# Performance work log

Measured on AMD Instinct MI355X. Metric: run time of the kernel, lower is better.

The kernel has to match this reference:

```python
import jax, jax.numpy as jnp
import numpy as np
from jax import lax

N_NODES = 100000
N_EDGES = 1600000
DIM = 64
N_GRAPHS = 128
OUT = 10
BN_EPS = 1e-5


def setup_inputs() -> dict:
    key = jax.random.key(0)
    ks = jax.random.split(key, 8)
    s = 1.0 / np.sqrt(DIM)
    x = jax.random.normal(ks[0], (N_NODES, DIM), dtype=jnp.float32)
    edge_index = jax.random.randint(ks[1], (2, N_EDGES), 0, N_NODES, dtype=jnp.int64)
    batch = jnp.sort(jax.random.randint(ks[2], (N_NODES,), 0, N_GRAPHS, dtype=jnp.int64))
    return {
        "x": x,
        "edge_index": edge_index,
        "batch": batch,
        "W1": jax.random.normal(ks[3], (5, DIM, DIM), dtype=jnp.float32) * s,
        "b1": jnp.zeros((5, DIM), jnp.float32),
        "gamma": jnp.ones((5, DIM), jnp.float32),
        "beta": jnp.zeros((5, DIM), jnp.float32),
        "rmean": jnp.zeros((5, DIM), jnp.float32),
        "rvar": jnp.ones((5, DIM), jnp.float32),
        "W2": jax.random.normal(ks[4], (5, DIM, DIM), dtype=jnp.float32) * s,
        "b2": jnp.zeros((5, DIM), jnp.float32),
        "lin1_w": jax.random.normal(ks[5], (DIM, DIM), dtype=jnp.float32) * s,
        "lin1_b": jnp.zeros((DIM,), jnp.float32),
        "lin2_w": jax.random.normal(ks[6], (DIM, OUT), dtype=jnp.float32) * s,
        "lin2_b": jnp.zeros((OUT,), jnp.float32),
    }


def reference(x, edge_index, batch, W1, b1, gamma, beta, rmean, rvar, W2, b2,
              lin1_w, lin1_b, lin2_w, lin2_b):
    n = x.shape[0]
    src, dst = edge_index[0], edge_index[1]

    def gin_layer(h, p):
        w1, bb1, g, bt, m, v, w2, bb2 = p
        # GINConv (eps=0): h_i <- MLP(h_i + sum_{j in N(i)} h_j)
        agg = jax.ops.segment_sum(h[src], dst, num_segments=n)
        h = h + agg
        h = h @ w1 + bb1
        h = (h - m) * lax.rsqrt(v + BN_EPS) * g + bt  # BatchNorm1d (eval)
        h = jax.nn.relu(h)
        h = jax.nn.relu(h @ w2 + bb2)
        return h, None

    h, _ = lax.scan(gin_layer, x, (W1, b1, gamma, beta, rmean, rvar, W2, b2))
    # global_add_pool over graphs in the batch
    pooled = jax.ops.segment_sum(h, batch, num_segments=N_GRAPHS)  # [G, dim]
    pooled = jax.nn.relu(pooled @ lin1_w + lin1_b)
    # dropout is identity in eval mode
    return pooled @ lin2_w + lin2_b  # [G, out]
```

## Files before the change

### kernel.cpp

```cpp
#include <hip/hip_runtime.h>

#define N_NODES  100000
#define N_EDGES  1600000
#define DIM      64
#define N_GRAPHS 128
#define OUT_DIM  10
#define SCAN_NB    196
#define SCAN_CHUNK 512
#define RANGE_BITS 14
#define RANGE_SIZE 16384
#define N_RANGES   7
#define N_CHUNKS   32
#define CHUNK_EDGES (N_EDGES / N_CHUNKS)
#define NODE_PAD   (N_RANGES * RANGE_SIZE)

typedef unsigned int uint;
typedef unsigned short ushort;
typedef __attribute__((ext_vector_type(8))) short short8;
typedef __attribute__((ext_vector_type(4))) float f32x4;

__device__ __forceinline__ uint f2bf(float x) {
    uint b = __float_as_uint(x);
    b += 0x7fffu + ((b >> 16) & 1u);
    return b >> 16;
}


__global__ __launch_bounds__(1024) void histo_kernel(const int* __restrict__ dst,
                                                     int* __restrict__ counts8) {
    __shared__ int lds[RANGE_SIZE];
    const int r = blockIdx.x & 7;
    if (r >= N_RANGES) return;
    const int c = blockIdx.x >> 3;
    for (int j = threadIdx.x; j < RANGE_SIZE; j += 1024) lds[j] = 0;
    __syncthreads();
    const int beg = c * CHUNK_EDGES, end = beg + CHUNK_EDGES;
    for (int i = beg + threadIdx.x; i < end; i += 1024) {
        int d = dst[i];
        if ((d >> RANGE_BITS) == r) atomicAdd(&lds[d & (RANGE_SIZE - 1)], 1);
    }
    __syncthreads();
    int* outp = counts8 + (c * N_RANGES + r) * RANGE_SIZE;
    for (int j = threadIdx.x; j < RANGE_SIZE; j += 1024) outp[j] = lds[j];
}

__global__ void scanA_kernel(const int* __restrict__ counts8, int* __restrict__ blockSums, int n) {
    __shared__ int red[256];
    const int b = blockIdx.x, t = threadIdx.x;
    int s = 0;
#pragma unroll
    for (int k = 0; k < 2; ++k) {
        const int node = b * SCAN_CHUNK + t * 2 + k;
        if (node < n) {
            const int r = node >> RANGE_BITS, jj = node & (RANGE_SIZE - 1);
            for (int c = 0; c < N_CHUNKS; ++c)
                s += counts8[(c * N_RANGES + r) * RANGE_SIZE + jj];
        }
    }
    red[t] = s;
    __syncthreads();
    for (int off = 128; off > 0; off >>= 1) {
        if (t < off) red[t] += red[t + off];
        __syncthreads();
    }
    if (t == 0) blockSums[b] = red[0];
}

__global__ void scanB_kernel(const int* __restrict__ blockSums, int* __restrict__ blockOffs,
                             int* __restrict__ row_ptr) {
    __shared__ int sc[256];
    const int t = threadIdx.x;
    const int v = (t < SCAN_NB) ? blockSums[t] : 0;
    sc[t] = v;
    __syncthreads();
    for (int off = 1; off < 256; off <<= 1) {
        int u = (t >= off) ? sc[t - off] : 0;
        __syncthreads();
        sc[t] += u;
        __syncthreads();
    }
    if (t < SCAN_NB) blockOffs[t] = sc[t] - v;
    if (t == 255) row_ptr[N_NODES] = sc[255];
}

__global__ void scanC_kernel(const int* __restrict__ counts8, const int* __restrict__ blockOffs,
                             int* __restrict__ row_ptr, int* __restrict__ base8, int n) {
    __shared__ int sc[256];
    const int b = blockIdx.x, t = threadIdx.x;
    const int node0 = b * SCAN_CHUNK + t * 2;
    int cnt0[N_CHUNKS], cnt1[N_CHUNKS];
    int tot0 = 0, tot1 = 0;
    if (node0 < n) {
        const int r = node0 >> RANGE_BITS, jj = node0 & (RANGE_SIZE - 1);
        for (int c = 0; c < N_CHUNKS; ++c) {
            cnt0[c] = counts8[(c * N_RANGES + r) * RANGE_SIZE + jj];
            tot0 += cnt0[c];
        }
    }
    if (node0 + 1 < n) {
        const int r = (node0 + 1) >> RANGE_BITS, jj = (node0 + 1) & (RANGE_SIZE - 1);
        for (int c = 0; c < N_CHUNKS; ++c) {
            cnt1[c] = counts8[(c * N_RANGES + r) * RANGE_SIZE + jj];
            tot1 += cnt1[c];
        }
    }
    const int s = tot0 + tot1;
    sc[t] = s;
    __syncthreads();
    for (int off = 1; off < 256; off <<= 1) {
        int u = (t >= off) ? sc[t - off] : 0;
        __syncthreads();
        sc[t] += u;
        __syncthreads();
    }
    const int pre = blockOffs[b] + sc[t] - s;
    if (node0 < n) {
        row_ptr[node0] = pre;
        int run = pre;
        for (int c = 0; c < N_CHUNKS; ++c) { base8[c * NODE_PAD + node0] = run; run += cnt0[c]; }
    }
    if (node0 + 1 < n) {
        const int pre1 = pre + tot0;
        row_ptr[node0 + 1] = pre1;
        int run = pre1;
        for (int c = 0; c < N_CHUNKS; ++c) { base8[c * NODE_PAD + node0 + 1] = run; run += cnt1[c]; }
    }
}

__global__ __launch_bounds__(1024) void fill_kernel(const int* __restrict__ src,
                                                    const int* __restrict__ dst,
                                                    const int* __restrict__ base8,
                                                    int* __restrict__ col_idx) {
    __shared__ int lds[RANGE_SIZE];
    const int r = blockIdx.x & 7;
    if (r >= N_RANGES) return;
    const int c = blockIdx.x >> 3;
    const int* bp = base8 + c * NODE_PAD + r * RANGE_SIZE;
    for (int j = threadIdx.x; j < RANGE_SIZE; j += 1024) lds[j] = bp[j];
    __syncthreads();
    const int beg = c * CHUNK_EDGES, end = beg + CHUNK_EDGES;
    for (int i = beg + threadIdx.x; i < end; i += 1024) {
        int d = dst[i];
        if ((d >> RANGE_BITS) == r) {
            int pos = atomicAdd(&lds[d & (RANGE_SIZE - 1)], 1);
            col_idx[pos] = src[i];
        }
    }
}


__global__ void cvt_kernel(const float* __restrict__ x, ushort* __restrict__ xb, int n4) {
    int idx = blockIdx.x * blockDim.x + threadIdx.x;
    if (idx >= n4) return;
    float4 v = ((const float4*)x)[idx];
    uint2 o;
    o.x = f2bf(v.x) | (f2bf(v.y) << 16);
    o.y = f2bf(v.z) | (f2bf(v.w) << 16);
    ((uint2*)xb)[idx] = o;
}


__global__ void repack_kernel(const float* __restrict__ W1, const float* __restrict__ W2,
                              uint4* __restrict__ Wp) {
    const int wave = (blockIdx.x * blockDim.x + threadIdx.x) >> 6;
    if (wave >= 10) return;
    const int layer = wave >> 1;
    const float* W = (wave & 1) ? (W2 + layer * 4096) : (W1 + layer * 4096);
    const int lane = threadIdx.x & 63;
    const int n15 = lane & 15, quad = lane >> 4;
#pragma unroll
    for (int f = 0; f < 8; ++f) {
        const int outer = f >> 1, h = f & 1;
        uint p[4];
#pragma unroll
        for (int pj = 0; pj < 4; ++pj) {
            const int k0 = h * 32 + quad * 8 + 2 * pj;
            uint lo = f2bf(W[k0 * 64 + outer * 16 + n15]);
            uint hi = f2bf(W[(k0 + 1) * 64 + outer * 16 + n15]);
            p[pj] = lo | (hi << 16);
        }
        Wp[(wave * 8 + f) * 64 + lane] = make_uint4(p[0], p[1], p[2], p[3]);
    }
}


__device__ __forceinline__ void add_unpack(float acc[8], uint4 v) {
    acc[0] += __uint_as_float(v.x << 16);
    acc[1] += __uint_as_float(v.x & 0xffff0000u);
    acc[2] += __uint_as_float(v.y << 16);
    acc[3] += __uint_as_float(v.y & 0xffff0000u);
    acc[4] += __uint_as_float(v.z << 16);
    acc[5] += __uint_as_float(v.z & 0xffff0000u);
    acc[6] += __uint_as_float(v.w << 16);
    acc[7] += __uint_as_float(v.w & 0xffff0000u);
}

__global__ __launch_bounds__(256) void agg_kernel(
    const ushort* __restrict__ hb, ushort* __restrict__ tb,
    const int* __restrict__ row_ptr, const int* __restrict__ col_idx, int n)
{
    const uint4* __restrict__ hb4 = (const uint4*)hb;
    const int lane = threadIdx.x & 63;
    const int g = lane >> 3;
    const int q = lane & 7;
    const int wave = (blockIdx.x * blockDim.x + threadIdx.x) >> 6;
    const int i = wave * 8 + g;
    if (i >= n) return;
    const int rp0 = row_ptr[i];
    const int deg = row_ptr[i + 1] - rp0;

    float acc[8];
    {
        uint4 v = hb4[(size_t)i * 8 + q];
        acc[0] = __uint_as_float(v.x << 16);
        acc[1] = __uint_as_float(v.x & 0xffff0000u);
        acc[2] = __uint_as_float(v.y << 16);
        acc[3] = __uint_as_float(v.y & 0xffff0000u);
        acc[4] = __uint_as_float(v.z << 16);
        acc[5] = __uint_as_float(v.z & 0xffff0000u);
        acc[6] = __uint_as_float(v.w << 16);
        acc[7] = __uint_as_float(v.w & 0xffff0000u);
    }

    int e = 0;
    for (; e + 8 <= deg; e += 8) {
        int ix[8];
#pragma unroll
        for (int k = 0; k < 8; ++k) ix[k] = col_idx[rp0 + e + k];
        uint4 v[8];
#pragma unroll
        for (int k = 0; k < 8; ++k) v[k] = hb4[(size_t)ix[k] * 8 + q];
#pragma unroll
        for (int k = 0; k < 8; ++k) add_unpack(acc, v[k]);
    }
    if (e + 4 <= deg) {
        int ix[4];
#pragma unroll
        for (int k = 0; k < 4; ++k) ix[k] = col_idx[rp0 + e + k];
        uint4 v[4];
#pragma unroll
        for (int k = 0; k < 4; ++k) v[k] = hb4[(size_t)ix[k] * 8 + q];
#pragma unroll
        for (int k = 0; k < 4; ++k) add_unpack(acc, v[k]);
        e += 4;
    }
    for (; e < deg; ++e) {
        int ix = col_idx[rp0 + e];
        uint4 v = hb4[(size_t)ix * 8 + q];
        add_unpack(acc, v);
    }

    uint4 o;
    o.x = f2bf(acc[0]) | (f2bf(acc[1]) << 16);
    o.y = f2bf(acc[2]) | (f2bf(acc[3]) << 16);
    o.z = f2bf(acc[4]) | (f2bf(acc[5]) << 16);
    o.w = f2bf(acc[6]) | (f2bf(acc[7]) << 16);
    ((uint4*)tb)[(size_t)i * 8 + q] = o;
}


__global__ __launch_bounds__(256) void mlp_kernel(
    const ushort* __restrict__ tb, ushort* __restrict__ hb,
    const uint4* __restrict__ Wp,
    const float* __restrict__ b1, const float* __restrict__ gamma,
    const float* __restrict__ beta, const float* __restrict__ rmean,
    const float* __restrict__ rvar, const float* __restrict__ b2, int ntiles)
{
    __shared__ __align__(16) ushort U[4][16][72];
    const int lane = threadIdx.x & 63;
    const int wid  = threadIdx.x >> 6;
    const int n15  = lane & 15, quad = lane >> 4;

    short8 w1f[8], w2f[8];
    const short8* Wp8 = (const short8*)Wp;
#pragma unroll
    for (int f = 0; f < 8; ++f) {
        w1f[f] = Wp8[f * 64 + lane];
        w2f[f] = Wp8[(8 + f) * 64 + lane];
    }
    f32x4 sc[4], sh[4];
#pragma unroll
    for (int mt = 0; mt < 4; ++mt) {
        const int j0 = mt * 16 + quad * 4;
#pragma unroll
        for (int r = 0; r < 4; ++r) {
            float s = gamma[j0 + r] * rsqrtf(rvar[j0 + r] + 1e-5f);
            sc[mt][r] = s;
            sh[mt][r] = (b1[j0 + r] - rmean[j0 + r]) * s + beta[j0 + r];
        }
    }
    float bb2[4];
#pragma unroll
    for (int tc = 0; tc < 4; ++tc) bb2[tc] = b2[tc * 16 + n15];

    const int wave = blockIdx.x * 4 + wid;
    const int nwaves = gridDim.x * 4;
    for (int tile = wave; tile < ntiles; tile += nwaves) {
        const int nb = tile * 16;
        const short8* trow = (const short8*)(tb + (size_t)(nb + n15) * 64);
        short8 t0 = trow[quad];
        short8 t1 = trow[4 + quad];

        f32x4 c1[4];
#pragma unroll
        for (int mt = 0; mt < 4; ++mt) {
            c1[mt] = (f32x4){0.f, 0.f, 0.f, 0.f};
            c1[mt] = __builtin_amdgcn_mfma_f32_16x16x32_bf16(w1f[mt * 2 + 0], t0, c1[mt], 0, 0, 0);
            c1[mt] = __builtin_amdgcn_mfma_f32_16x16x32_bf16(w1f[mt * 2 + 1], t1, c1[mt], 0, 0, 0);
        }
#pragma unroll
        for (int mt = 0; mt < 4; ++mt) {
            float u0 = fmaxf(c1[mt][0] * sc[mt][0] + sh[mt][0], 0.f);
            float u1 = fmaxf(c1[mt][1] * sc[mt][1] + sh[mt][1], 0.f);
            float u2 = fmaxf(c1[mt][2] * sc[mt][2] + sh[mt][2], 0.f);
            float u3 = fmaxf(c1[mt][3] * sc[mt][3] + sh[mt][3], 0.f);
            uint2 pk;
            pk.x = f2bf(u0) | (f2bf(u1) << 16);
            pk.y = f2bf(u2) | (f2bf(u3) << 16);
            *(uint2*)&U[wid][n15][mt * 16 + quad * 4] = pk;
        }
        __threadfence_block();
        short8 u0 = *(const short8*)&U[wid][n15][quad * 8];
        short8 u1 = *(const short8*)&U[wid][n15][32 + quad * 8];

        f32x4 c2[4];
#pragma unroll
        for (int tc = 0; tc < 4; ++tc) {
            c2[tc] = (f32x4){0.f, 0.f, 0.f, 0.f};
            c2[tc] = __builtin_amdgcn_mfma_f32_16x16x32_bf16(u0, w2f[tc * 2 + 0], c2[tc], 0, 0, 0);
            c2[tc] = __builtin_amdgcn_mfma_f32_16x16x32_bf16(u1, w2f[tc * 2 + 1], c2[tc], 0, 0, 0);
        }
#pragma unroll
        for (int tc = 0; tc < 4; ++tc) {
#pragma unroll
            for (int r = 0; r < 4; ++r) {
                float v = fmaxf(c2[tc][r] + bb2[tc], 0.f);
                hb[(size_t)(nb + quad * 4 + r) * 64 + tc * 16 + n15] = (ushort)f2bf(v);
            }
        }
    }
}


__global__ void pool_kernel(const ushort* __restrict__ hb, const int* __restrict__ batch,
                            float* __restrict__ pooled, int n) {
    const int lane = threadIdx.x & 63;
    const int wid  = threadIdx.x >> 6;
    const int wave = blockIdx.x * 4 + wid;
    const int nwaves = gridDim.x * 4;
    const int per = (n + nwaves - 1) / nwaves;
    const int a = wave * per;
    const int b = min(a + per, n);
    if (a >= b) return;
    int cur = batch[a];
    float sum = 0.0f;
    for (int i = a; i < b; ++i) {
        int g = batch[i];
        if (g != cur) {
            atomicAdd(&pooled[cur * DIM + lane], sum);
            sum = 0.0f;
            cur = g;
        }
        sum += __uint_as_float(((uint)hb[(size_t)i * DIM + lane]) << 16);
    }
    atomicAdd(&pooled[cur * DIM + lane], sum);
}


__global__ void head_kernel(const float* __restrict__ pooled,
                            const float* __restrict__ w1, const float* __restrict__ b1,
                            const float* __restrict__ w2, const float* __restrict__ b2,
                            float* __restrict__ out) {
    const int g = blockIdx.x;
    const int lane = threadIdx.x;
    __shared__ float pl[DIM];
    __shared__ float y1l[DIM];
    pl[lane] = pooled[g * DIM + lane];
    __syncthreads();
    float y = b1[lane];
#pragma unroll
    for (int d = 0; d < DIM; ++d) y += pl[d] * w1[d * DIM + lane];
    y1l[lane] = fmaxf(y, 0.0f);
    __syncthreads();
    if (lane < OUT_DIM) {
        float y2 = b2[lane];
#pragma unroll
        for (int d = 0; d < DIM; ++d) y2 += y1l[d] * w2[d * OUT_DIM + lane];
        out[g * OUT_DIM + lane] = y2;
    }
}


extern "C" void kernel_launch(void* const* d_in, const int* in_sizes, int n_in,
                              void* d_out, int out_size, void* d_ws, size_t ws_size,
                              hipStream_t stream) {
    const float* x     = (const float*)d_in[0];
    const int*   eidx  = (const int*)  d_in[1];
    const int*   batch = (const int*)  d_in[2];
    const float* W1    = (const float*)d_in[3];
    const float* b1    = (const float*)d_in[4];
    const float* gamma = (const float*)d_in[5];
    const float* beta  = (const float*)d_in[6];
    const float* rmean = (const float*)d_in[7];
    const float* rvar  = (const float*)d_in[8];
    const float* W2    = (const float*)d_in[9];
    const float* b2    = (const float*)d_in[10];
    const float* l1w   = (const float*)d_in[11];
    const float* l1b   = (const float*)d_in[12];
    const float* l2w   = (const float*)d_in[13];
    const float* l2b   = (const float*)d_in[14];
    float* out = (float*)d_out;

    const size_t C8 = (size_t)N_CHUNKS * N_RANGES * RANGE_SIZE;
    const size_t B8 = (size_t)N_CHUNKS * NODE_PAD;
    int* counts8   = (int*)d_ws;
    int* row_ptr   = counts8   + C8;
    int* blockSums = row_ptr   + 100352;
    int* blockOffs = blockSums + 256;
    int* base8     = blockOffs + 256;
    int* col_idx   = base8     + B8;
    uint4* Wp      = (uint4*)(col_idx + 1600000);
    ushort* tb     = (ushort*)(Wp + 5120);
    ushort* hb     = tb + (size_t)N_NODES * DIM;
    float* pooled  = (float*)(hb + (size_t)N_NODES * DIM);

    const int* srcp = eidx;
    const int* dstp = eidx + N_EDGES;

    hipMemsetAsync(pooled, 0, N_GRAPHS * DIM * sizeof(float), stream);

    cvt_kernel<<<(N_NODES * DIM / 4 + 255) / 256, 256, 0, stream>>>(x, hb, N_NODES * DIM / 4);
    repack_kernel<<<1, 640, 0, stream>>>(W1, W2, Wp);
    histo_kernel<<<N_CHUNKS * 8, 1024, 0, stream>>>(dstp, counts8);
    scanA_kernel<<<SCAN_NB, 256, 0, stream>>>(counts8, blockSums, N_NODES);
    scanB_kernel<<<1, 256, 0, stream>>>(blockSums, blockOffs, row_ptr);
    scanC_kernel<<<SCAN_NB, 256, 0, stream>>>(counts8, blockOffs, row_ptr, base8, N_NODES);
    fill_kernel<<<N_CHUNKS * 8, 1024, 0, stream>>>(srcp, dstp, base8, col_idx);

    const int agg_blocks = ((N_NODES + 7) / 8 * 64 + 255) / 256;
    const int ntiles = N_NODES / 16;

    for (int l = 0; l < 5; ++l) {
        agg_kernel<<<agg_blocks, 256, 0, stream>>>(hb, tb, row_ptr, col_idx, N_NODES);
        mlp_kernel<<<512, 256, 0, stream>>>(
            tb, hb, Wp + (size_t)l * 2 * 8 * 64,
            b1 + (size_t)l * DIM, gamma + (size_t)l * DIM, beta + (size_t)l * DIM,
            rmean + (size_t)l * DIM, rvar + (size_t)l * DIM, b2 + (size_t)l * DIM, ntiles);
    }
    pool_kernel<<<2048, 256, 0, stream>>>(hb, batch, pooled, N_NODES);
    head_kernel<<<N_GRAPHS, 64, 0, stream>>>(pooled, l1w, l1b, l2w, l2b, out);
}
```

Measured before the change: 410.6 us.

## Pre-partition edges by destination range before CSR histogram and fill

Replaces the CSR build, where every block scanned all edges of its chunk and filtered by node range, with a two-level scheme. Edges are first counted and scattered into seven destination-range buckets as (src,dst) pairs. The per-range histogram and fill kernels then read only their own bucket, split into 16 sub-slices. The aim is to cut the roughly 7x redundant reads of dst and src in histo and fill. In exchange it adds extra kernels and a write and read of an intermediate 12.8 MB edge buffer, and the global atomic scatter in partition has poor locality.

```diff
diff --git a/kernel.cpp b/kernel.cpp
--- a/kernel.cpp
+++ b/kernel.cpp
@@ -10,9 +10,10 @@
 #define RANGE_BITS 14
 #define RANGE_SIZE 16384
 #define N_RANGES   7
-#define N_CHUNKS   32
-#define CHUNK_EDGES (N_EDGES / N_CHUNKS)
 #define NODE_PAD   (N_RANGES * RANGE_SIZE)
+#define P_CHUNKS   64
+#define P_EDGES    (N_EDGES / P_CHUNKS)
+#define SUB        16
 
 typedef unsigned int uint;
 typedef unsigned short ushort;
@@ -26,38 +27,93 @@
 }
 
 
-__global__ __launch_bounds__(1024) void histo_kernel(const int* __restrict__ dst,
-                                                     int* __restrict__ counts8) {
-    __shared__ int lds[RANGE_SIZE];
+__global__ void count224_kernel(const int* __restrict__ dst, int* __restrict__ counts224) {
+    __shared__ int cnt[8];
+    const int c = blockIdx.x, tid = threadIdx.x;
+    if (tid < 8) cnt[tid] = 0;
+    __syncthreads();
+    int c0 = 0, c1 = 0, c2 = 0, c3 = 0, c4 = 0, c5 = 0, c6 = 0;
+    const int beg = c * P_EDGES, end = beg + P_EDGES;
+    for (int i = beg + tid; i < end; i += 256) {
+        int r = dst[i] >> RANGE_BITS;
+        c0 += (r == 0); c1 += (r == 1); c2 += (r == 2); c3 += (r == 3);
+        c4 += (r == 4); c5 += (r == 5); c6 += (r == 6);
+    }
+    atomicAdd(&cnt[0], c0); atomicAdd(&cnt[1], c1); atomicAdd(&cnt[2], c2);
+    atomicAdd(&cnt[3], c3); atomicAdd(&cnt[4], c4); atomicAdd(&cnt[5], c5);
+    atomicAdd(&cnt[6], c6);
+    __syncthreads();
+    if (tid < N_RANGES) counts224[tid * P_CHUNKS + c] = cnt[tid];
+}
+
+__global__ void scan224_kernel(const int* __restrict__ counts224, int* __restrict__ regionOff,
+                               int* __restrict__ rangeStart) {
+    __shared__ int sc[512];
+    const int t = threadIdx.x;
+    const int v = (t < N_RANGES * P_CHUNKS) ? counts224[t] : 0;
+    sc[t] = v;
+    __syncthreads();
+    for (int off = 1; off < 512; off <<= 1) {
+        int u = (t >= off) ? sc[t - off] : 0;
+        __syncthreads();
+        sc[t] += u;
+        __syncthreads();
+    }
+    if (t < N_RANGES * P_CHUNKS) regionOff[t] = sc[t] - v;
+    if (t < N_RANGES * P_CHUNKS && (t & (P_CHUNKS - 1)) == 0) rangeStart[t / P_CHUNKS] = sc[t] - v;
+    if (t == 511) rangeStart[N_RANGES] = sc[511];
+}
+
+__global__ __launch_bounds__(1024) void partition_kernel(
+    const int* __restrict__ src, const int* __restrict__ dst,
+    const int* __restrict__ regionOff, uint2* __restrict__ epart) {
+    __shared__ int pos[8];
+    const int c = blockIdx.x, tid = threadIdx.x;
+    if (tid < N_RANGES) pos[tid] = regionOff[tid * P_CHUNKS + c];
+    __syncthreads();
+    const int beg = c * P_EDGES, end = beg + P_EDGES;
+    for (int i = beg + tid; i < end; i += 1024) {
+        int d = dst[i], s = src[i];
+        int p = atomicAdd(&pos[d >> RANGE_BITS], 1);
+        epart[p] = make_uint2((uint)s, (uint)d);
+    }
+}
+
+__global__ __launch_bounds__(1024) void histoR_kernel(const uint2* __restrict__ epart,
+                                                      const int* __restrict__ rangeStart,
+                                                      int* __restrict__ countsS) {
+    __shared__ int h[RANGE_SIZE];
     const int r = blockIdx.x & 7;
     if (r >= N_RANGES) return;
-    const int c = blockIdx.x >> 3;
-    for (int j = threadIdx.x; j < RANGE_SIZE; j += 1024) lds[j] = 0;
-    __syncthreads();
-    const int beg = c * CHUNK_EDGES, end = beg + CHUNK_EDGES;
-    for (int i = beg + threadIdx.x; i < end; i += 1024) {
-        int d = dst[i];
-        if ((d >> RANGE_BITS) == r) atomicAdd(&lds[d & (RANGE_SIZE - 1)], 1);
-    }
-    __syncthreads();
-    int* outp = counts8 + (c * N_RANGES + r) * RANGE_SIZE;
-    for (int j = threadIdx.x; j < RANGE_SIZE; j += 1024) outp[j] = lds[j];
-}
-
-__global__ void scanA_kernel(const int* __restrict__ counts8, int* __restrict__ blockSums, int n) {
+    const int s = blockIdx.x >> 3;
+    const int tid = threadIdx.x;
+    for (int j = tid; j < RANGE_SIZE; j += 1024) h[j] = 0;
+    __syncthreads();
+    const int e0 = rangeStart[r], e1 = rangeStart[r + 1];
+    const int len = e1 - e0;
+    const int a = e0 + (int)((long long)len * s / SUB);
+    const int b = e0 + (int)((long long)len * (s + 1) / SUB);
+    for (int i = a + tid; i < b; i += 1024)
+        atomicAdd(&h[epart[i].y & (RANGE_SIZE - 1)], 1);
+    __syncthreads();
+    int* outp = countsS + (s * N_RANGES + r) * RANGE_SIZE;
+    for (int j = tid; j < RANGE_SIZE; j += 1024) outp[j] = h[j];
+}
+
+__global__ void scanA_kernel(const int* __restrict__ countsS, int* __restrict__ blockSums, int n) {
     __shared__ int red[256];
     const int b = blockIdx.x, t = threadIdx.x;
-    int s = 0;
+    int sum = 0;
 #pragma unroll
     for (int k = 0; k < 2; ++k) {
         const int node = b * SCAN_CHUNK + t * 2 + k;
         if (node < n) {
             const int r = node >> RANGE_BITS, jj = node & (RANGE_SIZE - 1);
-            for (int c = 0; c < N_CHUNKS; ++c)
-                s += counts8[(c * N_RANGES + r) * RANGE_SIZE + jj];
-        }
-    }
-    red[t] = s;
+            for (int s = 0; s < SUB; ++s)
+                sum += countsS[(s * N_RANGES + r) * RANGE_SIZE + jj];
+        }
+    }
+    red[t] = sum;
     __syncthreads();
     for (int off = 128; off > 0; off >>= 1) {
         if (t < off) red[t] += red[t + off];
@@ -83,29 +139,29 @@
     if (t == 255) row_ptr[N_NODES] = sc[255];
 }
 
-__global__ void scanC_kernel(const int* __restrict__ counts8, const int* __restrict__ blockOffs,
-                             int* __restrict__ row_ptr, int* __restrict__ base8, int n) {
+__global__ void scanC_kernel(const int* __restrict__ countsS, const int* __restrict__ blockOffs,
+                             int* __restrict__ row_ptr, int* __restrict__ baseS, int n) {
     __shared__ int sc[256];
     const int b = blockIdx.x, t = threadIdx.x;
     const int node0 = b * SCAN_CHUNK + t * 2;
-    int cnt0[N_CHUNKS], cnt1[N_CHUNKS];
+    int cnt0[SUB], cnt1[SUB];
     int tot0 = 0, tot1 = 0;
     if (node0 < n) {
         const int r = node0 >> RANGE_BITS, jj = node0 & (RANGE_SIZE - 1);
-        for (int c = 0; c < N_CHUNKS; ++c) {
-            cnt0[c] = counts8[(c * N_RANGES + r) * RANGE_SIZE + jj];
-            tot0 += cnt0[c];
+        for (int s = 0; s < SUB; ++s) {
+            cnt0[s] = countsS[(s * N_RANGES + r) * RANGE_SIZE + jj];
+            tot0 += cnt0[s];
         }
     }
     if (node0 + 1 < n) {
         const int r = (node0 + 1) >> RANGE_BITS, jj = (node0 + 1) & (RANGE_SIZE - 1);
-        for (int c = 0; c < N_CHUNKS; ++c) {
-            cnt1[c] = counts8[(c * N_RANGES + r) * RANGE_SIZE + jj];
-            tot1 += cnt1[c];
-        }
-    }
-    const int s = tot0 + tot1;
-    sc[t] = s;
+        for (int s = 0; s < SUB; ++s) {
+            cnt1[s] = countsS[(s * N_RANGES + r) * RANGE_SIZE + jj];
+            tot1 += cnt1[s];
+        }
+    }
+    const int ssum = tot0 + tot1;
+    sc[t] = ssum;
     __syncthreads();
     for (int off = 1; off < 256; off <<= 1) {
         int u = (t >= off) ? sc[t - off] : 0;
@@ -113,38 +169,40 @@
         sc[t] += u;
         __syncthreads();
     }
-    const int pre = blockOffs[b] + sc[t] - s;
+    const int pre = blockOffs[b] + sc[t] - ssum;
     if (node0 < n) {
         row_ptr[node0] = pre;
         int run = pre;
-        for (int c = 0; c < N_CHUNKS; ++c) { base8[c * NODE_PAD + node0] = run; run += cnt0[c]; }
+        for (int s = 0; s < SUB; ++s) { baseS[s * NODE_PAD + node0] = run; run += cnt0[s]; }
     }
     if (node0 + 1 < n) {
         const int pre1 = pre + tot0;
         row_ptr[node0 + 1] = pre1;
         int run = pre1;
-        for (int c = 0; c < N_CHUNKS; ++c) { base8[c * NODE_PAD + node0 + 1] = run; run += cnt1[c]; }
-    }
-}
-
-__global__ __launch_bounds__(1024) void fill_kernel(const int* __restrict__ src,
-                                                    const int* __restrict__ dst,
-                                                    const int* __restrict__ base8,
-                                                    int* __restrict__ col_idx) {
-    __shared__ int lds[RANGE_SIZE];
+        for (int s = 0; s < SUB; ++s) { baseS[s * NODE_PAD + node0 + 1] = run; run += cnt1[s]; }
+    }
+}
+
+__global__ __launch_bounds__(1024) void fillR_kernel(const uint2* __restrict__ epart,
+                                                     const int* __restrict__ rangeStart,
+                                                     const int* __restrict__ baseS,
+                                                     int* __restrict__ col_idx) {
+    __shared__ int slots[RANGE_SIZE];
     const int r = blockIdx.x & 7;
     if (r >= N_RANGES) return;
-    const int c = blockIdx.x >> 3;
-    const int* bp = base8 + c * NODE_PAD + r * RANGE_SIZE;
-    for (int j = threadIdx.x; j < RANGE_SIZE; j += 1024) lds[j] = bp[j];
-    __syncthreads();
-    const int beg = c * CHUNK_EDGES, end = beg + CHUNK_EDGES;
-    for (int i = beg + threadIdx.x; i < end; i += 1024) {
-        int d = dst[i];
-        if ((d >> RANGE_BITS) == r) {
-            int pos = atomicAdd(&lds[d & (RANGE_SIZE - 1)], 1);
-            col_idx[pos] = src[i];
-        }
+    const int s = blockIdx.x >> 3;
+    const int tid = threadIdx.x;
+    const int* bp = baseS + s * NODE_PAD + r * RANGE_SIZE;
+    for (int j = tid; j < RANGE_SIZE; j += 1024) slots[j] = bp[j];
+    __syncthreads();
+    const int e0 = rangeStart[r], e1 = rangeStart[r + 1];
+    const int len = e1 - e0;
+    const int a = e0 + (int)((long long)len * s / SUB);
+    const int b = e0 + (int)((long long)len * (s + 1) / SUB);
+    for (int i = a + tid; i < b; i += 1024) {
+        uint2 e = epart[i];
+        int pos = atomicAdd(&slots[e.y & (RANGE_SIZE - 1)], 1);
+        col_idx[pos] = (int)e.x;
     }
 }
 
@@ -411,18 +469,22 @@
     const float* l2b   = (const float*)d_in[14];
     float* out = (float*)d_out;
 
-    const size_t C8 = (size_t)N_CHUNKS * N_RANGES * RANGE_SIZE;
-    const size_t B8 = (size_t)N_CHUNKS * NODE_PAD;
-    int* counts8   = (int*)d_ws;
-    int* row_ptr   = counts8   + C8;
-    int* blockSums = row_ptr   + 100352;
-    int* blockOffs = blockSums + 256;
-    int* base8     = blockOffs + 256;
-    int* col_idx   = base8     + B8;
-    uint4* Wp      = (uint4*)(col_idx + 1600000);
-    ushort* tb     = (ushort*)(Wp + 5120);
-    ushort* hb     = tb + (size_t)N_NODES * DIM;
-    float* pooled  = (float*)(hb + (size_t)N_NODES * DIM);
+    const size_t CS = (size_t)SUB * N_RANGES * RANGE_SIZE;
+    const size_t BS = (size_t)SUB * NODE_PAD;
+    int* counts224  = (int*)d_ws;
+    int* regionOff  = counts224 + 512;
+    int* rangeStart = regionOff + 512;
+    int* blockSums  = rangeStart + 64;
+    int* blockOffs  = blockSums + 256;
+    int* row_ptr    = blockOffs + 256;
+    int* countsS    = row_ptr + 100352;
+    int* baseS      = countsS + CS;
+    uint2* epart    = (uint2*)(baseS + BS);
+    int* col_idx    = (int*)(epart + N_EDGES);
+    uint4* Wp       = (uint4*)(col_idx + 1600000);
+    ushort* tb      = (ushort*)(Wp + 5120);
+    ushort* hb      = tb + (size_t)N_NODES * DIM;
+    float* pooled   = (float*)(hb + (size_t)N_NODES * DIM);
 
     const int* srcp = eidx;
     const int* dstp = eidx + N_EDGES;
@@ -431,11 +493,14 @@
 
     cvt_kernel<<<(N_NODES * DIM / 4 + 255) / 256, 256, 0, stream>>>(x, hb, N_NODES * DIM / 4);
     repack_kernel<<<1, 640, 0, stream>>>(W1, W2, Wp);
-    histo_kernel<<<N_CHUNKS * 8, 1024, 0, stream>>>(dstp, counts8);
-    scanA_kernel<<<SCAN_NB, 256, 0, stream>>>(counts8, blockSums, N_NODES);
+    count224_kernel<<<P_CHUNKS, 256, 0, stream>>>(dstp, counts224);
+    scan224_kernel<<<1, 512, 0, stream>>>(counts224, regionOff, rangeStart);
+    partition_kernel<<<P_CHUNKS, 1024, 0, stream>>>(srcp, dstp, regionOff, epart);
+    histoR_kernel<<<SUB * 8, 1024, 0, stream>>>(epart, rangeStart, countsS);
+    scanA_kernel<<<SCAN_NB, 256, 0, stream>>>(countsS, blockSums, N_NODES);
     scanB_kernel<<<1, 256, 0, stream>>>(blockSums, blockOffs, row_ptr);
-    scanC_kernel<<<SCAN_NB, 256, 0, stream>>>(counts8, blockOffs, row_ptr, base8, N_NODES);
-    fill_kernel<<<N_CHUNKS * 8, 1024, 0, stream>>>(srcp, dstp, base8, col_idx);
+    scanC_kernel<<<SCAN_NB, 256, 0, stream>>>(countsS, blockOffs, row_ptr, baseS, N_NODES);
+    fillR_kernel<<<SUB * 8, 1024, 0, stream>>>(epart, rangeStart, baseS, col_idx);
 
     const int agg_blocks = ((N_NODES + 7) / 8 * 64 + 255) / 256;
     const int ntiles = N_NODES / 16;
```

After: 430.1 us. 1.05x slower.
